# Kernel tuning notes

Measured on AMD Instinct MI355X. Metric: run time of the kernel, lower is better.

The kernel has to match this reference:

```python
import jax, jax.numpy as jnp
import numpy as np

NUM_FORMULAS = 1024
INPUT_DIM = 256
BATCH = 2048


def setup_inputs() -> dict:
    key = jax.random.key(0)
    k_x, k_mu, k_sigma = jax.random.split(key, 3)
    inputs = jax.random.normal(k_x, (BATCH, INPUT_DIM), dtype=jnp.float32)
    # keras random_normal initializer default stddev = 0.05
    mu = 0.05 * jax.random.normal(k_mu, (NUM_FORMULAS, INPUT_DIM), dtype=jnp.float32)
    sigma = 0.05 * jax.random.normal(k_sigma, (1, NUM_FORMULAS, INPUT_DIM), dtype=jnp.float32)
    temperature = jnp.float32(2.0)
    return {"inputs": inputs, "mu": mu, "sigma": sigma, "temperature": temperature}


def reference(inputs, mu, sigma, temperature):
    # diff: (batch, num_formulas, dim)
    diff = inputs[:, None, :] - mu[None, :, :]
    # weighted L2 norm over feature dim -> (batch, num_formulas)
    dist = jnp.sqrt(jnp.sum(jnp.square(diff * sigma), axis=-1))
    loc = jnp.exp(-dist)
    # sigmoid-gated temperature, softmax over formulas (last axis)
    return jax.nn.softmax(jax.nn.sigmoid(temperature) * loc, axis=-1)
```

## Files before the change

### kernel.cpp

```cpp
#include <hip/hip_runtime.h>
#include <math.h>

#define NF 1024
#define DIM 256
#define BATCH 2048
#define K 512
#define BMF 16
#define GX (BATCH / BMF)
#define KS 32
#define NSTEP (K / KS)

#define WS_C_OFF (NF * K * 2)

typedef __attribute__((ext_vector_type(8))) short short8;
typedef __attribute__((ext_vector_type(4))) float f32x4;

__device__ __forceinline__ unsigned short f2bf(float f) {
    unsigned u = __float_as_uint(f);
    u += 0x7fffu + ((u >> 16) & 1u);
    return (unsigned short)(u >> 16);
}

__device__ __forceinline__ void gl_lds16(const ushort* g, ushort* l) {
    __builtin_amdgcn_global_load_lds(
        (const __attribute__((address_space(1))) void*)g,
        (__attribute__((address_space(3))) void*)l, 16, 0, 0);
}

__global__ __launch_bounds__(256) void k_prep(const float* __restrict__ mu,
                                              const float* __restrict__ sigma,
                                              unsigned int* __restrict__ Bb32,
                                              float* __restrict__ c) {
    const int t = threadIdx.x;
    const int f = blockIdx.x;
    const float m = mu[f * DIM + t];
    const float s = sigma[f * DIM + t];
    const float s2 = s * s;
    Bb32[(t >> 4) * (NF * 16) + f * 16 + (t & 15)] =
        (unsigned)f2bf(s2) | ((unsigned)f2bf(-2.0f * s2 * m) << 16);

    float cp = s2 * m * m;
    #pragma unroll
    for (int off = 32; off > 0; off >>= 1) cp += __shfl_down(cp, off, 64);
    __shared__ float red[4];
    const int lane = t & 63, wv = t >> 6;
    if (lane == 0) red[wv] = cp;
    __syncthreads();
    if (t == 0) c[f] = red[0] + red[1] + red[2] + red[3];
}

__global__ __launch_bounds__(512, 2) void k_full(const float* __restrict__ x,
                                                 const ushort* __restrict__ Bb,
                                                 const float* __restrict__ c,
                                                 const float* __restrict__ temp,
                                                 float* __restrict__ out) {
    const int t = threadIdx.x;
    const int w = t >> 6;
    const int lane = t & 63;
    const int m16 = lane & 15;
    const int q = lane >> 4;
    const int r0 = blockIdx.x * BMF;

    __shared__ __align__(16) ushort ldsA[BMF * K];
    __shared__ __align__(16) ushort ldsB[2][NF * KS];
    __shared__ float wsum[8][BMF];
    __shared__ float rowInv[BMF];

    #pragma unroll
    for (int h = 0; h < 2; ++h) {
        const int u = h * 512 + t;
        const int row = u >> 6, kc = u & 63;
        const float4 v = *(const float4*)&x[(r0 + row) * DIM + kc * 4];
        uint4 pk;
        pk.x = (unsigned)f2bf(v.x * v.x) | ((unsigned)f2bf(v.x) << 16);
        pk.y = (unsigned)f2bf(v.y * v.y) | ((unsigned)f2bf(v.y) << 16);
        pk.z = (unsigned)f2bf(v.z * v.z) | ((unsigned)f2bf(v.z) << 16);
        pk.w = (unsigned)f2bf(v.w * v.w) | ((unsigned)f2bf(v.w) << 16);
        *(uint4*)&ldsA[(row * 64 + (kc ^ (row & 7))) * 8] = pk;
    }

    f32x4 acc[8];
    #pragma unroll
    for (int ct = 0; ct < 8; ++ct) acc[ct] = (f32x4){0.f, 0.f, 0.f, 0.f};

    #pragma unroll
    for (int i = 0; i < 8; ++i) {
        const int u = i * 512 + t;
        gl_lds16(Bb + u * 8, &ldsB[0][u * 8]);
    }

    #pragma unroll 1
    for (int s = 0; s < NSTEP; ++s) {
        __syncthreads();
        if (s + 1 < NSTEP) {
            const ushort* src = Bb + (s + 1) * (NF * KS);
            ushort* dst = &ldsB[(s + 1) & 1][0];
            #pragma unroll
            for (int i = 0; i < 8; ++i) {
                const int u = i * 512 + t;
                gl_lds16(src + u * 8, dst + u * 8);
            }
        }
        const ushort* bcur = &ldsB[s & 1][0];
        const int kcq = s * 4 + q;
        const short8 av = *(const short8*)&ldsA[(m16 * 64 + (kcq ^ (m16 & 7))) * 8];
        #pragma unroll
        for (int ct = 0; ct < 8; ++ct) {
            const int f = w * 128 + ct * 16 + m16;
            const short8 bv = *(const short8*)&bcur[f * KS + q * 8];
            acc[ct] = __builtin_amdgcn_mfma_f32_16x16x32_bf16(av, bv, acc[ct], 0, 0, 0);
        }
    }

    const float g = 1.0f / (1.0f + __expf(-temp[0]));
    float s4[4] = {0.f, 0.f, 0.f, 0.f};
    #pragma unroll
    for (int ct = 0; ct < 8; ++ct) {
        const float cn = c[w * 128 + ct * 16 + m16];
        #pragma unroll
        for (int i = 0; i < 4; ++i) {
            const float dist2 = acc[ct][i] + cn;
            const float dist = sqrtf(fmaxf(dist2, 0.0f));
            const float p = __expf(g * __expf(-dist));
            acc[ct][i] = p;
            s4[i] += p;
        }
    }
    #pragma unroll
    for (int i = 0; i < 4; ++i) {
        #pragma unroll
        for (int mask = 1; mask < 16; mask <<= 1)
            s4[i] += __shfl_xor(s4[i], mask, 64);
    }
    if (m16 == 0) {
        #pragma unroll
        for (int i = 0; i < 4; ++i) wsum[w][q * 4 + i] = s4[i];
    }
    __syncthreads();
    if (t < BMF) {
        float ssum = 0.f;
        #pragma unroll
        for (int ww = 0; ww < 8; ++ww) ssum += wsum[ww][t];
        rowInv[t] = 1.0f / ssum;
    }
    __syncthreads();

    float inv[4];
    #pragma unroll
    for (int i = 0; i < 4; ++i) inv[i] = rowInv[q * 4 + i];
    #pragma unroll
    for (int ct = 0; ct < 8; ++ct) {
        const int fcol = w * 128 + ct * 16 + m16;
        #pragma unroll
        for (int i = 0; i < 4; ++i)
            out[(r0 + q * 4 + i) * NF + fcol] = acc[ct][i] * inv[i];
    }
}

extern "C" void kernel_launch(void* const* d_in, const int* in_sizes, int n_in,
                              void* d_out, int out_size, void* d_ws, size_t ws_size,
                              hipStream_t stream) {
    const float* x     = (const float*)d_in[0];
    const float* mu    = (const float*)d_in[1];
    const float* sigma = (const float*)d_in[2];
    const float* temp  = (const float*)d_in[3];
    float* out = (float*)d_out;

    char* ws = (char*)d_ws;
    ushort* Bb = (ushort*)ws;
    float*  c  = (float*)(ws + WS_C_OFF);

    k_prep<<<NF, 256, 0, stream>>>(mu, sigma, (unsigned int*)Bb, c);
    k_full<<<GX, 512, 0, stream>>>(x, Bb, c, temp, out);
}
```

Baseline: 85.78 us.

## Split formula columns across blocks and normalize softmax in a separate pass

The main kernel now splits the 1024 formulas into 4 column chunks over a second grid dimension. This gives 512 blocks of 256 threads instead of 128 blocks of 512, with a smaller LDS footprint to raise occupancy. Unnormalized exponentials and per-chunk row partial sums are written out, and a new normalization kernel rescales each output row. The prep kernel is vectorized with a new B layout chunked per column group. The trade-off is an extra kernel launch, a second read and write of the full output, and each chunk-block re-converting the x tile.

```diff
diff --git a/kernel.cpp b/kernel.cpp
--- a/kernel.cpp
+++ b/kernel.cpp
@@ -6,11 +6,13 @@
 #define BATCH 2048
 #define K 512
 #define BMF 16
-#define GX (BATCH / BMF)
+#define NCC 4
+#define CF (NF / NCC)
 #define KS 32
 #define NSTEP (K / KS)
 
-#define WS_C_OFF (NF * K * 2)
+#define WS_C_OFF  (NF * K * 2)
+#define WS_RP_OFF (WS_C_OFF + NF * 4)
 
 typedef __attribute__((ext_vector_type(8))) short short8;
 typedef __attribute__((ext_vector_type(4))) float f32x4;
@@ -29,46 +31,57 @@
 
 __global__ __launch_bounds__(256) void k_prep(const float* __restrict__ mu,
                                               const float* __restrict__ sigma,
-                                              unsigned int* __restrict__ Bb32,
+                                              uint4* __restrict__ Bb4,
                                               float* __restrict__ c) {
     const int t = threadIdx.x;
-    const int f = blockIdx.x;
-    const float m = mu[f * DIM + t];
-    const float s = sigma[f * DIM + t];
-    const float s2 = s * s;
-    Bb32[(t >> 4) * (NF * 16) + f * 16 + (t & 15)] =
-        (unsigned)f2bf(s2) | ((unsigned)f2bf(-2.0f * s2 * m) << 16);
+    const int f = blockIdx.x * 4 + (t >> 6);
+    const int sq = t & 63;
+    const float4 mv = *(const float4*)&mu[f * DIM + sq * 4];
+    const float4 sv = *(const float4*)&sigma[f * DIM + sq * 4];
 
-    float cp = s2 * m * m;
+    uint4 pk; float cp = 0.f;
+    {
+        const float s2x = sv.x * sv.x;
+        pk.x = (unsigned)f2bf(s2x) | ((unsigned)f2bf(-2.0f * s2x * mv.x) << 16);
+        cp += s2x * mv.x * mv.x;
+        const float s2y = sv.y * sv.y;
+        pk.y = (unsigned)f2bf(s2y) | ((unsigned)f2bf(-2.0f * s2y * mv.y) << 16);
+        cp += s2y * mv.y * mv.y;
+        const float s2z = sv.z * sv.z;
+        pk.z = (unsigned)f2bf(s2z) | ((unsigned)f2bf(-2.0f * s2z * mv.z) << 16);
+        cp += s2z * mv.z * mv.z;
+        const float s2w = sv.w * sv.w;
+        pk.w = (unsigned)f2bf(s2w) | ((unsigned)f2bf(-2.0f * s2w * mv.w) << 16);
+        cp += s2w * mv.w * mv.w;
+    }
+    Bb4[(f >> 8) * 16384 + (sq >> 2) * 1024 + (sq & 3) * 256 + (f & 255)] = pk;
+
     #pragma unroll
     for (int off = 32; off > 0; off >>= 1) cp += __shfl_down(cp, off, 64);
-    __shared__ float red[4];
-    const int lane = t & 63, wv = t >> 6;
-    if (lane == 0) red[wv] = cp;
-    __syncthreads();
-    if (t == 0) c[f] = red[0] + red[1] + red[2] + red[3];
+    if ((t & 63) == 0) c[f] = cp;
 }
 
-__global__ __launch_bounds__(512, 2) void k_full(const float* __restrict__ x,
+__global__ __launch_bounds__(256, 3) void k_main(const float* __restrict__ x,
                                                  const ushort* __restrict__ Bb,
                                                  const float* __restrict__ c,
                                                  const float* __restrict__ temp,
-                                                 float* __restrict__ out) {
+                                                 float* __restrict__ out,
+                                                 float* __restrict__ rowPartial) {
     const int t = threadIdx.x;
     const int w = t >> 6;
     const int lane = t & 63;
     const int m16 = lane & 15;
     const int q = lane >> 4;
     const int r0 = blockIdx.x * BMF;
+    const int cc = blockIdx.y;
 
     __shared__ __align__(16) ushort ldsA[BMF * K];
-    __shared__ __align__(16) ushort ldsB[2][NF * KS];
-    __shared__ float wsum[8][BMF];
-    __shared__ float rowInv[BMF];
+    __shared__ __align__(16) ushort ldsB[2][CF * KS];
+    __shared__ float wsum[4][BMF];
 
     #pragma unroll
-    for (int h = 0; h < 2; ++h) {
-        const int u = h * 512 + t;
+    for (int h = 0; h < 4; ++h) {
+        const int u = h * 256 + t;
         const int row = u >> 6, kc = u & 63;
         const float4 v = *(const float4*)&x[(r0 + row) * DIM + kc * 4];
         uint4 pk;
@@ -79,25 +92,27 @@
         *(uint4*)&ldsA[(row * 64 + (kc ^ (row & 7))) * 8] = pk;
     }
 
-    f32x4 acc[8];
+    f32x4 acc[4];
     #pragma unroll
-    for (int ct = 0; ct < 8; ++ct) acc[ct] = (f32x4){0.f, 0.f, 0.f, 0.f};
+    for (int ct = 0; ct < 4; ++ct) acc[ct] = (f32x4){0.f, 0.f, 0.f, 0.f};
+
+    const ushort* bsrc = Bb + cc * (CF * K);
 
     #pragma unroll
-    for (int i = 0; i < 8; ++i) {
-        const int u = i * 512 + t;
-        gl_lds16(Bb + u * 8, &ldsB[0][u * 8]);
+    for (int i = 0; i < 4; ++i) {
+        const int u = i * 256 + t;
+        gl_lds16(bsrc + u * 8, &ldsB[0][u * 8]);
     }
 
     #pragma unroll 1
     for (int s = 0; s < NSTEP; ++s) {
         __syncthreads();
         if (s + 1 < NSTEP) {
-            const ushort* src = Bb + (s + 1) * (NF * KS);
+            const ushort* src = bsrc + (s + 1) * (CF * KS);
             ushort* dst = &ldsB[(s + 1) & 1][0];
             #pragma unroll
-            for (int i = 0; i < 8; ++i) {
-                const int u = i * 512 + t;
+            for (int i = 0; i < 4; ++i) {
+                const int u = i * 256 + t;
                 gl_lds16(src + u * 8, dst + u * 8);
             }
         }
@@ -105,9 +120,9 @@
         const int kcq = s * 4 + q;
         const short8 av = *(const short8*)&ldsA[(m16 * 64 + (kcq ^ (m16 & 7))) * 8];
         #pragma unroll
-        for (int ct = 0; ct < 8; ++ct) {
-            const int f = w * 128 + ct * 16 + m16;
-            const short8 bv = *(const short8*)&bcur[f * KS + q * 8];
+        for (int ct = 0; ct < 4; ++ct) {
+            const int fl = w * 64 + ct * 16 + m16;
+            const short8 bv = *(const short8*)&bcur[q * (CF * 8) + fl * 8];
             acc[ct] = __builtin_amdgcn_mfma_f32_16x16x32_bf16(av, bv, acc[ct], 0, 0, 0);
         }
     }
@@ -115,14 +130,15 @@
     const float g = 1.0f / (1.0f + __expf(-temp[0]));
     float s4[4] = {0.f, 0.f, 0.f, 0.f};
     #pragma unroll
-    for (int ct = 0; ct < 8; ++ct) {
-        const float cn = c[w * 128 + ct * 16 + m16];
+    for (int ct = 0; ct < 4; ++ct) {
+        const int fcol = cc * CF + w * 64 + ct * 16 + m16;
+        const float cn = c[fcol];
         #pragma unroll
         for (int i = 0; i < 4; ++i) {
             const float dist2 = acc[ct][i] + cn;
             const float dist = sqrtf(fmaxf(dist2, 0.0f));
             const float p = __expf(g * __expf(-dist));
-            acc[ct][i] = p;
+            out[(r0 + q * 4 + i) * NF + fcol] = p;
             s4[i] += p;
         }
     }
@@ -137,24 +153,21 @@
         for (int i = 0; i < 4; ++i) wsum[w][q * 4 + i] = s4[i];
     }
     __syncthreads();
-    if (t < BMF) {
-        float ssum = 0.f;
-        #pragma unroll
-        for (int ww = 0; ww < 8; ++ww) ssum += wsum[ww][t];
-        rowInv[t] = 1.0f / ssum;
-    }
-    __syncthreads();
+    if (t < BMF)
+        rowPartial[cc * BATCH + r0 + t] =
+            (wsum[0][t] + wsum[1][t]) + (wsum[2][t] + wsum[3][t]);
+}
 
-    float inv[4];
-    #pragma unroll
-    for (int i = 0; i < 4; ++i) inv[i] = rowInv[q * 4 + i];
-    #pragma unroll
-    for (int ct = 0; ct < 8; ++ct) {
-        const int fcol = w * 128 + ct * 16 + m16;
-        #pragma unroll
-        for (int i = 0; i < 4; ++i)
-            out[(r0 + q * 4 + i) * NF + fcol] = acc[ct][i] * inv[i];
-    }
+__global__ __launch_bounds__(256) void k_norm(float* __restrict__ out,
+                                              const float* __restrict__ rowPartial) {
+    const int row = blockIdx.x;
+    const float ssum = (rowPartial[row] + rowPartial[BATCH + row]) +
+                       (rowPartial[2 * BATCH + row] + rowPartial[3 * BATCH + row]);
+    const float inv = 1.0f / ssum;
+    float4* o4 = (float4*)(out + row * NF);
+    float4 v = o4[threadIdx.x];
+    v.x *= inv; v.y *= inv; v.z *= inv; v.w *= inv;
+    o4[threadIdx.x] = v;
 }
 
 extern "C" void kernel_launch(void* const* d_in, const int* in_sizes, int n_in,
@@ -167,9 +180,14 @@
     float* out = (float*)d_out;
 
     char* ws = (char*)d_ws;
-    ushort* Bb = (ushort*)ws;
-    float*  c  = (float*)(ws + WS_C_OFF);
+    ushort* Bb         = (ushort*)ws;
+    float*  c          = (float*)(ws + WS_C_OFF);
+    float*  rowPartial = (float*)(ws + WS_RP_OFF);
 
-    k_prep<<<NF, 256, 0, stream>>>(mu, sigma, (unsigned int*)Bb, c);
-    k_full<<<GX, 512, 0, stream>>>(x, Bb, c, temp, out);
+    k_prep<<<NF / 4, 256, 0, stream>>>(mu, sigma, (uint4*)Bb, c);
+
+    dim3 g2(BATCH / BMF, NCC);
+    k_main<<<g2, 256, 0, stream>>>(x, Bb, c, temp, out, rowPartial);
+
+    k_norm<<<BATCH, 256, 0, stream>>>(out, rowPartial);
 }
```

After: 82.70 us. 3.6% less time.
